# Kernel optimization log

Hardware: AMD Instinct MI355X
Metric: run time of the kernel (lower is better)

Reference implementation:

```python
import jax, jax.numpy as jnp
import numpy as np

N, E, G = 20000, 100000, 64          # nodes, edges, graphs in batch
IN, HID = 63, 128                    # in_feat, hidden_feat (per-head dim)
HEADS = (8, 8, 8)                    # num_heads per GATv2 layer
NCLS = 18
EPS = 1e-5


def setup_inputs() -> dict:
    key = jax.random.key(0)
    ks = list(jax.random.split(key, 48))
    it = iter(ks)
    nrm = lambda shape, s=0.05: jax.random.normal(next(it), shape, jnp.float32) * s

    inp = {
        "h": jax.random.normal(next(it), (N, IN), jnp.float32),
        "src": jax.random.randint(next(it), (E,), 0, N, dtype=jnp.int32),
        "dst": jax.random.randint(next(it), (E,), 0, N, dtype=jnp.int32),
        "gid": jnp.sort(jax.random.randint(next(it), (N,), 0, G, dtype=jnp.int32)),
    }
    dims = [(IN, HEADS[0] * HID), (HEADS[0] * HID, HEADS[1] * HID), (HEADS[1] * HID, HEADS[2] * HID)]
    for l, (din, dout) in enumerate(dims, 1):
        H = HEADS[l - 1]
        inp[f"w_src{l}"] = nrm((din, dout))
        inp[f"b_src{l}"] = jnp.zeros((dout,), jnp.float32)
        inp[f"w_dst{l}"] = nrm((din, dout))
        inp[f"b_dst{l}"] = jnp.zeros((dout,), jnp.float32)
        inp[f"attn{l}"] = nrm((H, HID))
        inp[f"bias{l}"] = jnp.zeros((dout,), jnp.float32)
        inp[f"gamma{l}"] = jnp.ones((dout,), jnp.float32)
        inp[f"beta{l}"] = jnp.zeros((dout,), jnp.float32)
    inp["fc1_w"] = nrm((HEADS[2] * HID, HID * 8))   # 1024 -> 1024 (hidden_feat*num_heads -> hidden_feat? see note)
    inp["fc1_b"] = jnp.zeros((HID * 8,), jnp.float32)
    inp["fc2_w"] = nrm((HID * 8, 1024))
    inp["fc2_b"] = jnp.zeros((1024,), jnp.float32)
    inp["fc3_w"] = nrm((1024, NCLS))
    inp["fc3_b"] = jnp.zeros((NCLS,), jnp.float32)
    return inp


def _gatv2(h, w_src, b_src, w_dst, b_dst, attn, bias, src, dst):
    """DGL GATv2Conv forward (dropouts are identity in eval mode)."""
    H, D = attn.shape
    fs = (h @ w_src + b_src).reshape(N, H, D)   # [N,H,D]
    fd = (h @ w_dst + b_dst).reshape(N, H, D)
    e = jax.nn.leaky_relu(fs[src] + fd[dst], 0.2)          # [E,H,D], GATv2 negative_slope=0.2
    sc = jnp.einsum('ehd,hd->eh', e, attn)                 # [E,H] attention logits
    m = jax.ops.segment_max(sc, dst, num_segments=N)       # segment-softmax over in-edges
    m = jnp.where(jnp.isfinite(m), m, 0.0)                 # guard isolated nodes
    ex = jnp.exp(sc - m[dst])
    den = jax.ops.segment_sum(ex, dst, num_segments=N)
    alpha = ex / den[dst]                                  # [E,H]
    out = jax.ops.segment_sum(alpha[..., None] * fs[src], dst, num_segments=N)  # [N,H,D]
    return out.reshape(N, H * D) + bias


def _bn(x, gamma, beta):
    mu = x.mean(0)
    var = x.var(0)  # biased, as torch BN uses for normalization
    return (x - mu) * jax.lax.rsqrt(var + EPS) * gamma + beta


def _lrelu(x):
    return jax.nn.leaky_relu(x, 0.01)  # torch F.leaky_relu default slope


def reference(h, src, dst, gid,
              w_src1, b_src1, w_dst1, b_dst1, attn1, bias1, gamma1, beta1,
              w_src2, b_src2, w_dst2, b_dst2, attn2, bias2, gamma2, beta2,
              w_src3, b_src3, w_dst3, b_dst3, attn3, bias3, gamma3, beta3,
              fc1_w, fc1_b, fc2_w, fc2_b, fc3_w, fc3_b):
    x = _lrelu(_bn(_gatv2(h, w_src1, b_src1, w_dst1, b_dst1, attn1, bias1, src, dst), gamma1, beta1))
    x = _lrelu(_bn(_gatv2(x, w_src2, b_src2, w_dst2, b_dst2, attn2, bias2, src, dst), gamma2, beta2))
    x = _lrelu(_bn(_gatv2(x, w_src3, b_src3, w_dst3, b_dst3, attn3, bias3, src, dst), gamma3, beta3))
    # AvgPooling: mean over nodes of each graph
    cnt = jax.ops.segment_sum(jnp.ones((N,), x.dtype), gid, num_segments=G)
    hg = jax.ops.segment_sum(x, gid, num_segments=G) / jnp.maximum(cnt, 1.0)[:, None]  # [G, 1024]
    z = _lrelu(hg @ fc1_w + fc1_b)
    z = _lrelu(z @ fc2_w + fc2_b)
    return z @ fc3_w + fc3_b  # [G, 18]
```

## Files before the change

kernel.cpp:

```cpp
#include <hip/hip_runtime.h>
#include <math.h>

#define N_NODES 20000
#define N_PAD   20096
#define N_EDGES 100000
#define N_GRAPHS 64
#define IN_F 63
#define NHEAD 8
#define F 1024
#define NCLS 18
#define BN_EPS 1e-5f
#define BN_CHUNKS 256

typedef __attribute__((ext_vector_type(8))) _Float16 half8v;
typedef __attribute__((ext_vector_type(4))) _Float16 half4v;
typedef __attribute__((ext_vector_type(4))) float f32x4;

__global__ void k_zero_i32(int* __restrict__ p, int n) {
    int i = blockIdx.x * blockDim.x + threadIdx.x;
    if (i < n) p[i] = 0;
}

__global__ void k_copy_i32(int* __restrict__ d, const int* __restrict__ s, int n) {
    int i = blockIdx.x * blockDim.x + threadIdx.x;
    if (i < n) d[i] = s[i];
}

__global__ void k_count(const int* __restrict__ dst, int* __restrict__ cnt) {
    int i = blockIdx.x * blockDim.x + threadIdx.x;
    if (i < N_EDGES) atomicAdd(&cnt[dst[i]], 1);
}

__global__ void k_scan(const int* __restrict__ cnt, int* __restrict__ off) {
    __shared__ int tsum[256];
    const int CH = (N_NODES + 255) / 256;
    int t = threadIdx.x;
    int s = 0;
    for (int i = 0; i < CH; ++i) {
        int idx = t * CH + i;
        if (idx < N_NODES) s += cnt[idx];
    }
    tsum[t] = s;
    __syncthreads();
    if (t == 0) {
        int acc = 0;
        for (int i = 0; i < 256; ++i) { int v = tsum[i]; tsum[i] = acc; acc += v; }
    }
    __syncthreads();
    int run = tsum[t];
    for (int i = 0; i < CH; ++i) {
        int idx = t * CH + i;
        if (idx < N_NODES) { off[idx] = run; run += cnt[idx]; }
    }
    if (t == 255) off[N_NODES] = run;
}

__global__ void k_fill(const int* __restrict__ dst, int* __restrict__ cursor,
                       int* __restrict__ csr_e) {
    int i = blockIdx.x * blockDim.x + threadIdx.x;
    if (i < N_EDGES) {
        int p = atomicAdd(&cursor[dst[i]], 1);
        csr_e[p] = i;
    }
}

__global__ void k_sort_buckets(const int* __restrict__ off, int* __restrict__ csr_e) {
    int n = blockIdx.x * blockDim.x + threadIdx.x;
    if (n >= N_NODES) return;
    int b = off[n], e = off[n + 1];
    for (int i = b + 1; i < e; ++i) {
        int v = csr_e[i];
        int j = i - 1;
        while (j >= b && csr_e[j] > v) { csr_e[j + 1] = csr_e[j]; --j; }
        csr_e[j + 1] = v;
    }
}

__global__ void k_gstart(const int* __restrict__ gid, int* __restrict__ gstart) {
    int g = blockIdx.x * blockDim.x + threadIdx.x;
    if (g > N_GRAPHS) return;
    int lo = 0, hi = N_NODES;
    while (lo < hi) {
        int mid = (lo + hi) >> 1;
        if (gid[mid] < g) lo = mid + 1; else hi = mid;
    }
    gstart[g] = lo;
}

__global__ void k_cvt_h(const float* __restrict__ h, _Float16* __restrict__ xh) {
    int idx = blockIdx.x * 256 + threadIdx.x;
    if (idx >= N_PAD * 64) return;
    int m = idx >> 6, k = idx & 63;
    float v = (m < N_NODES && k < IN_F) ? h[m * IN_F + k] : 0.f;
    xh[idx] = (_Float16)v;
}

__global__ void k_zero_pad(_Float16* __restrict__ xh) {
    int idx = blockIdx.x * 256 + threadIdx.x;
    const int total = (N_PAD - N_NODES) * F;
    if (idx < total) xh[(size_t)N_NODES * F + idx] = (_Float16)0.f;
}

__global__ void k_cvt_w2(const float* __restrict__ W0, _Float16* __restrict__ o0,
                         const float* __restrict__ W1, _Float16* __restrict__ o1,
                         int K, int Kpad) {
    const float* W = blockIdx.z ? W1 : W0;
    _Float16* wh = blockIdx.z ? o1 : o0;
    __shared__ float t[32][33];
    int kt = blockIdx.x * 32, nt = blockIdx.y * 32;
    int tx = threadIdx.x & 31, ty = threadIdx.x >> 5;
#pragma unroll
    for (int j = 0; j < 4; ++j) {
        int k = kt + ty + j * 8;
        t[ty + j * 8][tx] = (k < K) ? W[(size_t)k * F + nt + tx] : 0.f;
    }
    __syncthreads();
#pragma unroll
    for (int j = 0; j < 4; ++j) {
        int n = nt + ty + j * 8;
        wh[(size_t)n * Kpad + kt + tx] = (_Float16)t[tx][ty + j * 8];
    }
}

#define AS1C(p) ((const __attribute__((address_space(1))) void*)(p))
#define AS3(p)  ((__attribute__((address_space(3))) void*)(p))

template <int KPAD>
__launch_bounds__(256, 2)
__global__ void k_gemm_dual(const _Float16* __restrict__ A,
                            const _Float16* __restrict__ Bs, const _Float16* __restrict__ Bd,
                            const float* __restrict__ bias_s, const float* __restrict__ bias_d,
                            _Float16* __restrict__ Cs, _Float16* __restrict__ Cd) {
    __shared__ _Float16 lds[3][3][128 * 32];
    const int l = threadIdx.x & 63, w = threadIdx.x >> 6;

    const int orig = blockIdx.y * 8 + blockIdx.x;
    const int wg = (orig & 7) * (N_PAD / 128) + (orig >> 3);
    const int by = wg >> 3, bx = wg & 7;

    const int srow = w * 16 + (l >> 2);
    const int schunk = ((l & 3) ^ ((l >> 2) & 3) ^ ((l >> 4) & 3)) << 3;
    const _Float16* gA  = A  + (size_t)(by * 128 + srow) * KPAD + schunk;
    const _Float16* gBs = Bs + (size_t)(bx * 128 + srow) * KPAD + schunk;
    const _Float16* gBd = Bd + (size_t)(bx * 128 + srow) * KPAD + schunk;
    const size_t jstep = (size_t)64 * KPAD;

    const int wr = (w >> 1) * 64, wc = (w & 1) * 64;
    const int frow = l & 15;
    const int kbyte = ((l & 3) ^ ((l >> 2) & 3) ^ ((l >> 4) & 3)) << 4;

    f32x4 accS[4][4], accD[4][4];
    const f32x4 fzero = {0.f, 0.f, 0.f, 0.f};
#pragma unroll
    for (int i = 0; i < 4; ++i)
#pragma unroll
        for (int j = 0; j < 4; ++j) { accS[i][j] = fzero; accD[i][j] = fzero; }

    auto stage = [&](int b, int t) {
        const int k0 = t * 32;
        char* dA  = (char*)&lds[b][0][0] + w * 1024;
        char* dBs = (char*)&lds[b][1][0] + w * 1024;
        char* dBd = (char*)&lds[b][2][0] + w * 1024;
#pragma unroll
        for (int j = 0; j < 2; ++j) {
            __builtin_amdgcn_global_load_lds(AS1C(gA  + k0 + j * jstep), AS3(dA  + j * 4096), 16, 0, 0);
            __builtin_amdgcn_global_load_lds(AS1C(gBs + k0 + j * jstep), AS3(dBs + j * 4096), 16, 0, 0);
            __builtin_amdgcn_global_load_lds(AS1C(gBd + k0 + j * jstep), AS3(dBd + j * 4096), 16, 0, 0);
        }
    };

    auto compute = [&](int b) {
        const char* lA  = (const char*)&lds[b][0][0];
        const char* lBs = (const char*)&lds[b][1][0];
        const char* lBd = (const char*)&lds[b][2][0];
        half8v a[4];
#pragma unroll
        for (int mi = 0; mi < 4; ++mi)
            a[mi] = *(const half8v*)(lA + (wr + mi * 16 + frow) * 64 + kbyte);
#pragma unroll
        for (int ni = 0; ni < 4; ++ni) {
            const int rb = (wc + ni * 16 + frow) * 64 + kbyte;
            half8v bs = *(const half8v*)(lBs + rb);
            half8v bd = *(const half8v*)(lBd + rb);
#pragma unroll
            for (int mi = 0; mi < 4; ++mi) {
                accS[mi][ni] = __builtin_amdgcn_mfma_f32_16x16x32_f16(a[mi], bs, accS[mi][ni], 0, 0, 0);
                accD[mi][ni] = __builtin_amdgcn_mfma_f32_16x16x32_f16(a[mi], bd, accD[mi][ni], 0, 0, 0);
            }
        }
    };

    constexpr int NT = KPAD / 32;
    stage(0, 0);
    if (NT > 1) stage(1, 1);
#pragma unroll 1
    for (int t = 0; t < NT; ++t) {
        if (t == NT - 1) asm volatile("s_waitcnt vmcnt(0)" ::: "memory");
        else             asm volatile("s_waitcnt vmcnt(6)" ::: "memory");
        __builtin_amdgcn_s_barrier();
        __builtin_amdgcn_sched_barrier(0);
        if (t + 2 < NT) stage((t + 2) % 3, t + 2);
        compute(t % 3);
    }

    const int crow0 = by * 128 + wr + (l >> 4) * 4;
    const int ccol = bx * 128 + wc + (l & 15);
    float bS[4], bD[4];
#pragma unroll
    for (int ni = 0; ni < 4; ++ni) { bS[ni] = bias_s[ccol + ni * 16]; bD[ni] = bias_d[ccol + ni * 16]; }
#pragma unroll
    for (int mi = 0; mi < 4; ++mi) {
#pragma unroll
        for (int r = 0; r < 4; ++r) {
            int row = crow0 + mi * 16 + r;
            if (row < N_NODES) {
#pragma unroll
                for (int ni = 0; ni < 4; ++ni) {
                    int col = ccol + ni * 16;
                    Cs[(size_t)row * F + col] = (_Float16)(accS[mi][ni][r] + bS[ni]);
                    Cd[(size_t)row * F + col] = (_Float16)(accD[mi][ni][r] + bD[ni]);
                }
            }
        }
    }
}

__launch_bounds__(128)
__global__ void k_gat(const _Float16* __restrict__ fs, const _Float16* __restrict__ fd,
                      const int* __restrict__ off, const int* __restrict__ csr_e,
                      const int* __restrict__ src, const float* __restrict__ attn,
                      const float* __restrict__ bias, _Float16* __restrict__ y16) {
    __shared__ int s_src[128];
    const int n = blockIdx.x;
    const int t = threadIdx.x;
    const int b = off[n], e = off[n + 1];

    half8v fdv8 = *(const half8v*)(fd + (size_t)n * F + t * 8);
    float fdv[8], av[8];
    const float4 a0 = *(const float4*)(attn + (t >> 4) * 128 + (t & 15) * 8);
    const float4 a1 = *(const float4*)(attn + (t >> 4) * 128 + (t & 15) * 8 + 4);
    av[0] = a0.x; av[1] = a0.y; av[2] = a0.z; av[3] = a0.w;
    av[4] = a1.x; av[5] = a1.y; av[6] = a1.z; av[7] = a1.w;
#pragma unroll
    for (int j = 0; j < 8; ++j) fdv[j] = (float)fdv8[j];

    float m = -1e30f, den = 0.f;
    float acc[8] = {0.f, 0.f, 0.f, 0.f, 0.f, 0.f, 0.f, 0.f};

    for (int c0 = b; c0 < e; c0 += 128) {
        int ncur = e - c0; if (ncur > 128) ncur = 128;
        __syncthreads();
        if (t < ncur) s_src[t] = src[csr_e[c0 + t]];
        __syncthreads();
        for (int i = 0; i < ncur; ++i) {
            int s = s_src[i];
            half8v fsv8 = *(const half8v*)(fs + (size_t)s * F + t * 8);
            float f[8];
            float p = 0.f;
#pragma unroll
            for (int j = 0; j < 8; ++j) {
                f[j] = (float)fsv8[j];
                float v = f[j] + fdv[j];
                v = v > 0.f ? v : 0.2f * v;
                p += v * av[j];
            }
            p += __shfl_xor(p, 1);
            p += __shfl_xor(p, 2);
            p += __shfl_xor(p, 4);
            p += __shfl_xor(p, 8);
            float mn = fmaxf(m, p);
            float so = __expf(m - mn);
            float wexp = __expf(p - mn);
            den = den * so + wexp;
#pragma unroll
            for (int j = 0; j < 8; ++j) acc[j] = acc[j] * so + wexp * f[j];
            m = mn;
        }
    }
    float inv = (e > b) ? 1.f / den : 0.f;
    const float4 b0 = *(const float4*)(bias + t * 8);
    const float4 b1 = *(const float4*)(bias + t * 8 + 4);
    float bb[8] = {b0.x, b0.y, b0.z, b0.w, b1.x, b1.y, b1.z, b1.w};
    half8v o;
#pragma unroll
    for (int j = 0; j < 8; ++j) o[j] = (_Float16)(acc[j] * inv + bb[j]);
    *(half8v*)(y16 + (size_t)n * F + t * 8) = o;
}

__global__ void k_bnpart(const _Float16* __restrict__ y16, float* __restrict__ part) {
    const int ROWS = (N_NODES + BN_CHUNKS - 1) / BN_CHUNKS;
    int blk = blockIdx.x;
    int t = threadIdx.x;
    int r0 = blk * ROWS;
    int r1 = r0 + ROWS; if (r1 > N_NODES) r1 = N_NODES;
    float sx = 0.f, sy = 0.f, sz = 0.f, sw = 0.f;
    float qx = 0.f, qy = 0.f, qz = 0.f, qw = 0.f;
    for (int r = r0; r < r1; ++r) {
        half4v v = *(const half4v*)(y16 + (size_t)r * F + t * 4);
        float vx = (float)v.x, vy = (float)v.y, vz = (float)v.z, vw = (float)v.w;
        sx += vx; sy += vy; sz += vz; sw += vw;
        qx += vx * vx; qy += vy * vy; qz += vz * vz; qw += vw * vw;
    }
    float4 s4; s4.x = sx; s4.y = sy; s4.z = sz; s4.w = sw;
    float4 q4; q4.x = qx; q4.y = qy; q4.z = qz; q4.w = qw;
    *(float4*)(part + (size_t)blk * (2 * F) + t * 4) = s4;
    *(float4*)(part + (size_t)blk * (2 * F) + F + t * 4) = q4;
}

__global__ void k_bnfin(const float* __restrict__ part, const float* __restrict__ gamma,
                        const float* __restrict__ beta, float* __restrict__ scale,
                        float* __restrict__ shift) {
    int c = blockIdx.x * blockDim.x + threadIdx.x;
    if (c >= F) return;
    float s = 0.f, q = 0.f;
    for (int b = 0; b < BN_CHUNKS; ++b) {
        s += part[(size_t)b * (2 * F) + c];
        q += part[(size_t)b * (2 * F) + F + c];
    }
    float mu = s / (float)N_NODES;
    float var = q / (float)N_NODES - mu * mu;
    float sc = gamma[c] * rsqrtf(var + BN_EPS);
    scale[c] = sc;
    shift[c] = beta[c] - mu * sc;
}

__global__ void k_bnapply(const _Float16* __restrict__ y16, const float* __restrict__ scale,
                          const float* __restrict__ shift, float* __restrict__ x,
                          _Float16* __restrict__ xh, int mode) {
    int i = blockIdx.x * blockDim.x + threadIdx.x;
    if (i >= N_NODES * (F / 4)) return;
    int c4 = (i & (F / 4 - 1)) * 4;
    half4v v = ((const half4v*)y16)[i];
    float4 o;
    o.x = (float)v.x * scale[c4 + 0] + shift[c4 + 0];
    o.y = (float)v.y * scale[c4 + 1] + shift[c4 + 1];
    o.z = (float)v.z * scale[c4 + 2] + shift[c4 + 2];
    o.w = (float)v.w * scale[c4 + 3] + shift[c4 + 3];
    o.x = o.x > 0.f ? o.x : 0.01f * o.x;
    o.y = o.y > 0.f ? o.y : 0.01f * o.y;
    o.z = o.z > 0.f ? o.z : 0.01f * o.z;
    o.w = o.w > 0.f ? o.w : 0.01f * o.w;
    if (mode == 0) {
        half4v h4;
        h4.x = (_Float16)o.x; h4.y = (_Float16)o.y;
        h4.z = (_Float16)o.z; h4.w = (_Float16)o.w;
        *(half4v*)&xh[(size_t)i * 4] = h4;
    } else {
        ((float4*)x)[i] = o;
    }
}

__global__ void k_pool(const float* __restrict__ x, const int* __restrict__ gstart,
                       _Float16* __restrict__ hg16) {
    int g = blockIdx.y;
    int col = blockIdx.x * 256 + threadIdx.x;
    int r0 = gstart[g], r1 = gstart[g + 1];
    float s = 0.f;
    for (int r = r0; r < r1; ++r) s += x[(size_t)r * F + col];
    float inv = (r1 > r0) ? 1.f / (float)(r1 - r0) : 0.f;
    hg16[(size_t)g * F + col] = (_Float16)(s * inv);
}

__launch_bounds__(256)
__global__ void k_mlp_mfma(const _Float16* __restrict__ A16, const _Float16* __restrict__ Bt,
                           const float* __restrict__ bias, _Float16* __restrict__ out16,
                           float* __restrict__ out32, int mode) {
    const int l = threadIdx.x & 63, w = threadIdx.x >> 6;
    const int bx = blockIdx.x;
    const int fko = (l >> 4) * 8;

    const _Float16* pa = A16 + (size_t)(w * 16 + (l & 15)) * 1024 + fko;
    const _Float16* pb = Bt + (size_t)(bx * 64 + (l & 15)) * 1024 + fko;

    f32x4 acc[4];
    const f32x4 fzero = {0.f, 0.f, 0.f, 0.f};
#pragma unroll
    for (int ni = 0; ni < 4; ++ni) acc[ni] = fzero;

#pragma unroll 4
    for (int k0 = 0; k0 < 1024; k0 += 32) {
        half8v a = *(const half8v*)(pa + k0);
#pragma unroll
        for (int ni = 0; ni < 4; ++ni) {
            half8v b = *(const half8v*)(pb + (size_t)ni * 16 * 1024 + k0);
            acc[ni] = __builtin_amdgcn_mfma_f32_16x16x32_f16(a, b, acc[ni], 0, 0, 0);
        }
    }

    const int row0 = w * 16 + (l >> 4) * 4;
    const int col0 = bx * 64 + (l & 15);
#pragma unroll
    for (int ni = 0; ni < 4; ++ni) {
        int col = col0 + ni * 16;
        float bb = bias[col];
#pragma unroll
        for (int r = 0; r < 4; ++r) {
            float v = acc[ni][r] + bb;
            v = v > 0.f ? v : 0.01f * v;
            if (mode == 0) out16[(size_t)(row0 + r) * 1024 + col] = (_Float16)v;
            else out32[(size_t)(row0 + r) * 1024 + col] = v;
        }
    }
}

__global__ void k_fc3(const float* __restrict__ z2, const float* __restrict__ W,
                      const float* __restrict__ b, float* __restrict__ out) {
    int gw = (blockIdx.x * blockDim.x + threadIdx.x) >> 6;
    int lane = threadIdx.x & 63;
    if (gw >= N_GRAPHS * NCLS) return;
    int row = gw / NCLS, col = gw - row * NCLS;
    float s = 0.f;
    for (int k = lane; k < 1024; k += 64) s += z2[(size_t)row * 1024 + k] * W[(size_t)k * NCLS + col];
#pragma unroll
    for (int o = 32; o; o >>= 1) s += __shfl_down(s, o);
    if (lane == 0) out[(size_t)row * NCLS + col] = s + b[col];
}

extern "C" void kernel_launch(void* const* d_in, const int* in_sizes, int n_in,
                              void* d_out, int out_size, void* d_ws, size_t ws_size,
                              hipStream_t stream) {
    const float* h = (const float*)d_in[0];
    const int* src = (const int*)d_in[1];
    const int* dst = (const int*)d_in[2];
    const int* gid = (const int*)d_in[3];

    const float *w_src[3], *b_src[3], *w_dst[3], *b_dst[3], *attn[3], *bias[3], *gamma[3], *beta[3];
    for (int l = 0; l < 3; ++l) {
        int base = 4 + l * 8;
        w_src[l] = (const float*)d_in[base + 0];
        b_src[l] = (const float*)d_in[base + 1];
        w_dst[l] = (const float*)d_in[base + 2];
        b_dst[l] = (const float*)d_in[base + 3];
        attn[l]  = (const float*)d_in[base + 4];
        bias[l]  = (const float*)d_in[base + 5];
        gamma[l] = (const float*)d_in[base + 6];
        beta[l]  = (const float*)d_in[base + 7];
    }
    const float* fc1_w = (const float*)d_in[28];
    const float* fc1_b = (const float*)d_in[29];
    const float* fc2_w = (const float*)d_in[30];
    const float* fc2_b = (const float*)d_in[31];
    const float* fc3_w = (const float*)d_in[32];
    const float* fc3_b = (const float*)d_in[33];

    char* base = (char*)d_ws;
    size_t o = 0;
    auto carve = [&](size_t bytes) -> char* {
        char* p = base + o;
        o += (bytes + 255) & ~(size_t)255;
        return p;
    };
    _Float16* fs16 = (_Float16*)carve((size_t)N_NODES * F * 2);
    _Float16* fd16 = (_Float16*)carve((size_t)N_NODES * F * 2);
    _Float16* y16 = (_Float16*)carve((size_t)N_NODES * F * 2);
    float* x32 = (float*)carve((size_t)N_NODES * F * 4);
    _Float16* xh = (_Float16*)carve((size_t)N_PAD * F * 2);
    _Float16* wsh = (_Float16*)carve((size_t)F * F * 2);
    _Float16* wdh = (_Float16*)carve((size_t)F * F * 2);
    _Float16* fc1h = (_Float16*)carve((size_t)F * F * 2);
    _Float16* fc2h = (_Float16*)carve((size_t)F * F * 2);
    int* cnt = (int*)carve((size_t)N_NODES * 4);
    int* off = (int*)carve((size_t)(N_NODES + 1) * 4);
    int* cursor = (int*)carve((size_t)N_NODES * 4);
    int* csr_e = (int*)carve((size_t)N_EDGES * 4);
    float* part = (float*)carve((size_t)BN_CHUNKS * 2 * F * 4);
    float* scale = (float*)carve(F * 4);
    float* shift = (float*)carve(F * 4);
    int* gstart = (int*)carve((N_GRAPHS + 1) * 4);
    _Float16* hg16 = (_Float16*)carve((size_t)N_GRAPHS * F * 2);
    _Float16* z1h = (_Float16*)carve((size_t)N_GRAPHS * F * 2);
    float* z2 = (float*)carve((size_t)N_GRAPHS * F * 4);
    (void)ws_size;

    k_zero_i32<<<(N_NODES + 255) / 256, 256, 0, stream>>>(cnt, N_NODES);
    k_count<<<(N_EDGES + 255) / 256, 256, 0, stream>>>(dst, cnt);
    k_scan<<<1, 256, 0, stream>>>(cnt, off);
    k_copy_i32<<<(N_NODES + 255) / 256, 256, 0, stream>>>(cursor, off, N_NODES);
    k_fill<<<(N_EDGES + 255) / 256, 256, 0, stream>>>(dst, cursor, csr_e);
    k_sort_buckets<<<(N_NODES + 255) / 256, 256, 0, stream>>>(off, csr_e);
    k_gstart<<<1, 128, 0, stream>>>(gid, gstart);

    k_cvt_h<<<(N_PAD * 64 + 255) / 256, 256, 0, stream>>>(h, xh);
    k_zero_pad<<<((N_PAD - N_NODES) * F + 255) / 256, 256, 0, stream>>>(xh);
    k_cvt_w2<<<dim3(F / 32, F / 32, 2), 256, 0, stream>>>(fc1_w, fc1h, fc2_w, fc2h, F, F);

    const dim3 ggrid(8, N_PAD / 128);
    for (int l = 0; l < 3; ++l) {
        const int K = (l == 0) ? IN_F : F;
        const int Kp = (l == 0) ? 64 : F;
        k_cvt_w2<<<dim3(Kp / 32, F / 32, 2), 256, 0, stream>>>(w_src[l], wsh, w_dst[l], wdh, K, Kp);
        if (Kp == 64)
            k_gemm_dual<64><<<ggrid, 256, 0, stream>>>(xh, wsh, wdh, b_src[l], b_dst[l], fs16, fd16);
        else
            k_gemm_dual<1024><<<ggrid, 256, 0, stream>>>(xh, wsh, wdh, b_src[l], b_dst[l], fs16, fd16);
        k_gat<<<N_NODES, 128, 0, stream>>>(fs16, fd16, off, csr_e, src, attn[l], bias[l], y16);
        k_bnpart<<<BN_CHUNKS, 256, 0, stream>>>(y16, part);
        k_bnfin<<<F / 256, 256, 0, stream>>>(part, gamma[l], beta[l], scale, shift);
        k_bnapply<<<(N_NODES * (F / 4) + 255) / 256, 256, 0, stream>>>(
            y16, scale, shift, x32, xh, (l == 2) ? 1 : 0);
    }

    k_pool<<<dim3(4, N_GRAPHS), 256, 0, stream>>>(x32, gstart, hg16);
    k_mlp_mfma<<<16, 256, 0, stream>>>(hg16, fc1h, fc1_b, z1h, nullptr, 0);
    k_mlp_mfma<<<16, 256, 0, stream>>>(z1h, fc2h, fc2_b, nullptr, z2, 1);
    k_fc3<<<(N_GRAPHS * NCLS * 64 + 255) / 256, 256, 0, stream>>>(z2, fc3_w, fc3_b, (float*)d_out);
}
```

Before: 793.2 us.

## Merge preprocessing kernels, batch weight conversion, simplify GEMM pipeline, pool from fp16

Several launches are folded together. The gstart search moves into the scan kernel, the cursor copy is replaced by a second counter array, and all six 1024x1024 weight conversions run in one launch. The dual GEMM loses its templated triple-buffered global_load_lds pipeline in favour of a single-buffered 64-wide K loop with an XOR swizzle and two __syncthreads per step, which may expose load latency. The last layer now writes fp16 activations only, and pooling reads them, so the fp32 activation buffer and its writes are gone at a small precision cost.

Measured after the change: 773.2 us. -2.5%, faster.

```diff
diff --git a/kernel.cpp b/kernel.cpp
--- a/kernel.cpp
+++ b/kernel.cpp
@@ -21,17 +21,13 @@
     if (i < n) p[i] = 0;
 }
 
-__global__ void k_copy_i32(int* __restrict__ d, const int* __restrict__ s, int n) {
-    int i = blockIdx.x * blockDim.x + threadIdx.x;
-    if (i < n) d[i] = s[i];
-}
-
 __global__ void k_count(const int* __restrict__ dst, int* __restrict__ cnt) {
     int i = blockIdx.x * blockDim.x + threadIdx.x;
     if (i < N_EDGES) atomicAdd(&cnt[dst[i]], 1);
 }
 
-__global__ void k_scan(const int* __restrict__ cnt, int* __restrict__ off) {
+__global__ void k_scan(const int* __restrict__ cnt, int* __restrict__ off,
+                       const int* __restrict__ gid, int* __restrict__ gstart) {
     __shared__ int tsum[256];
     const int CH = (N_NODES + 255) / 256;
     int t = threadIdx.x;
@@ -53,14 +49,23 @@
         if (idx < N_NODES) { off[idx] = run; run += cnt[idx]; }
     }
     if (t == 255) off[N_NODES] = run;
-}
-
-__global__ void k_fill(const int* __restrict__ dst, int* __restrict__ cursor,
-                       int* __restrict__ csr_e) {
+    if (t <= N_GRAPHS) {
+        int lo = 0, hi = N_NODES;
+        while (lo < hi) {
+            int mid = (lo + hi) >> 1;
+            if (gid[mid] < t) lo = mid + 1; else hi = mid;
+        }
+        gstart[t] = lo;
+    }
+}
+
+__global__ void k_fill(const int* __restrict__ dst, const int* __restrict__ off,
+                       int* __restrict__ fcnt, int* __restrict__ csr_e) {
     int i = blockIdx.x * blockDim.x + threadIdx.x;
     if (i < N_EDGES) {
-        int p = atomicAdd(&cursor[dst[i]], 1);
-        csr_e[p] = i;
+        int d = dst[i];
+        int p = atomicAdd(&fcnt[d], 1);
+        csr_e[off[d] + p] = i;
     }
 }
 
@@ -76,17 +81,6 @@
     }
 }
 
-__global__ void k_gstart(const int* __restrict__ gid, int* __restrict__ gstart) {
-    int g = blockIdx.x * blockDim.x + threadIdx.x;
-    if (g > N_GRAPHS) return;
-    int lo = 0, hi = N_NODES;
-    while (lo < hi) {
-        int mid = (lo + hi) >> 1;
-        if (gid[mid] < g) lo = mid + 1; else hi = mid;
-    }
-    gstart[g] = lo;
-}
-
 __global__ void k_cvt_h(const float* __restrict__ h, _Float16* __restrict__ xh) {
     int idx = blockIdx.x * 256 + threadIdx.x;
     if (idx >= N_PAD * 64) return;
@@ -122,32 +116,67 @@
     }
 }
 
+__global__ void k_cvt_w6(const float* __restrict__ a0, _Float16* __restrict__ b0,
+                         const float* __restrict__ a1, _Float16* __restrict__ b1,
+                         const float* __restrict__ a2, _Float16* __restrict__ b2,
+                         const float* __restrict__ a3, _Float16* __restrict__ b3,
+                         const float* __restrict__ a4, _Float16* __restrict__ b4,
+                         const float* __restrict__ a5, _Float16* __restrict__ b5) {
+    const float* W; _Float16* wh;
+    switch (blockIdx.z) {
+        case 0: W = a0; wh = b0; break;
+        case 1: W = a1; wh = b1; break;
+        case 2: W = a2; wh = b2; break;
+        case 3: W = a3; wh = b3; break;
+        case 4: W = a4; wh = b4; break;
+        default: W = a5; wh = b5; break;
+    }
+    __shared__ float t[32][33];
+    int kt = blockIdx.x * 32, nt = blockIdx.y * 32;
+    int tx = threadIdx.x & 31, ty = threadIdx.x >> 5;
+#pragma unroll
+    for (int j = 0; j < 4; ++j) {
+        int k = kt + ty + j * 8;
+        t[ty + j * 8][tx] = W[(size_t)k * F + nt + tx];
+    }
+    __syncthreads();
+#pragma unroll
+    for (int j = 0; j < 4; ++j) {
+        int n = nt + ty + j * 8;
+        wh[(size_t)n * F + kt + tx] = (_Float16)t[tx][ty + j * 8];
+    }
+}
+
 #define AS1C(p) ((const __attribute__((address_space(1))) void*)(p))
 #define AS3(p)  ((__attribute__((address_space(3))) void*)(p))
 
-template <int KPAD>
 __launch_bounds__(256, 2)
 __global__ void k_gemm_dual(const _Float16* __restrict__ A,
                             const _Float16* __restrict__ Bs, const _Float16* __restrict__ Bd,
                             const float* __restrict__ bias_s, const float* __restrict__ bias_d,
-                            _Float16* __restrict__ Cs, _Float16* __restrict__ Cd) {
-    __shared__ _Float16 lds[3][3][128 * 32];
-    const int l = threadIdx.x & 63, w = threadIdx.x >> 6;
+                            _Float16* __restrict__ Cs, _Float16* __restrict__ Cd, int Kpad) {
+    __shared__ _Float16 lds[24576];
+    const int tid = threadIdx.x;
+    const int l = tid & 63, w = tid >> 6;
 
     const int orig = blockIdx.y * 8 + blockIdx.x;
     const int wg = (orig & 7) * (N_PAD / 128) + (orig >> 3);
     const int by = wg >> 3, bx = wg & 7;
 
-    const int srow = w * 16 + (l >> 2);
-    const int schunk = ((l & 3) ^ ((l >> 2) & 3) ^ ((l >> 4) & 3)) << 3;
-    const _Float16* gA  = A  + (size_t)(by * 128 + srow) * KPAD + schunk;
-    const _Float16* gBs = Bs + (size_t)(bx * 128 + srow) * KPAD + schunk;
-    const _Float16* gBd = Bd + (size_t)(bx * 128 + srow) * KPAD + schunk;
-    const size_t jstep = (size_t)64 * KPAD;
+    const int grow = w * 32 + (l >> 3);
+    const int gcol = ((l & 7) ^ (l >> 3)) << 3;
+    const size_t rstep = (size_t)8 * Kpad;
+    const _Float16* gA = A + (size_t)(by * 128 + grow) * Kpad + gcol;
+    const _Float16* gBs = Bs + (size_t)(bx * 128 + grow) * Kpad + gcol;
+    const _Float16* gBd = Bd + (size_t)(bx * 128 + grow) * Kpad + gcol;
+    char* sA = (char*)lds + w * 4096;
+    char* sBs = (char*)lds + 16384 + w * 4096;
+    char* sBd = (char*)lds + 32768 + w * 4096;
 
     const int wr = (w >> 1) * 64, wc = (w & 1) * 64;
     const int frow = l & 15;
-    const int kbyte = ((l & 3) ^ ((l >> 2) & 3) ^ ((l >> 4) & 3)) << 4;
+    const int swz = (l & 7) << 4;
+    const int kbase = (l >> 4) * 16;
 
     f32x4 accS[4][4], accD[4][4];
     const f32x4 fzero = {0.f, 0.f, 0.f, 0.f};
@@ -156,51 +185,38 @@
 #pragma unroll
         for (int j = 0; j < 4; ++j) { accS[i][j] = fzero; accD[i][j] = fzero; }
 
-    auto stage = [&](int b, int t) {
-        const int k0 = t * 32;
-        char* dA  = (char*)&lds[b][0][0] + w * 1024;
-        char* dBs = (char*)&lds[b][1][0] + w * 1024;
-        char* dBd = (char*)&lds[b][2][0] + w * 1024;
-#pragma unroll
-        for (int j = 0; j < 2; ++j) {
-            __builtin_amdgcn_global_load_lds(AS1C(gA  + k0 + j * jstep), AS3(dA  + j * 4096), 16, 0, 0);
-            __builtin_amdgcn_global_load_lds(AS1C(gBs + k0 + j * jstep), AS3(dBs + j * 4096), 16, 0, 0);
-            __builtin_amdgcn_global_load_lds(AS1C(gBd + k0 + j * jstep), AS3(dBd + j * 4096), 16, 0, 0);
-        }
-    };
-
-    auto compute = [&](int b) {
-        const char* lA  = (const char*)&lds[b][0][0];
-        const char* lBs = (const char*)&lds[b][1][0];
-        const char* lBd = (const char*)&lds[b][2][0];
-        half8v a[4];
-#pragma unroll
-        for (int mi = 0; mi < 4; ++mi)
-            a[mi] = *(const half8v*)(lA + (wr + mi * 16 + frow) * 64 + kbyte);
-#pragma unroll
-        for (int ni = 0; ni < 4; ++ni) {
-            const int rb = (wc + ni * 16 + frow) * 64 + kbyte;
-            half8v bs = *(const half8v*)(lBs + rb);
-            half8v bd = *(const half8v*)(lBd + rb);
+    for (int k0 = 0; k0 < Kpad; k0 += 64) {
+#pragma unroll
+        for (int j = 0; j < 4; ++j) {
+            __builtin_amdgcn_global_load_lds(AS1C(gA + j * rstep), AS3(sA + j * 1024), 16, 0, 0);
+            __builtin_amdgcn_global_load_lds(AS1C(gBs + j * rstep), AS3(sBs + j * 1024), 16, 0, 0);
+            __builtin_amdgcn_global_load_lds(AS1C(gBd + j * rstep), AS3(sBd + j * 1024), 16, 0, 0);
+        }
+        gA += 64; gBs += 64; gBd += 64;
+        __syncthreads();
+
+#pragma unroll
+        for (int kk = 0; kk < 2; ++kk) {
+            const int kb = (kk * 64 + kbase) ^ swz;
+            half8v a[4];
 #pragma unroll
             for (int mi = 0; mi < 4; ++mi) {
-                accS[mi][ni] = __builtin_amdgcn_mfma_f32_16x16x32_f16(a[mi], bs, accS[mi][ni], 0, 0, 0);
-                accD[mi][ni] = __builtin_amdgcn_mfma_f32_16x16x32_f16(a[mi], bd, accD[mi][ni], 0, 0, 0);
+                int row = wr + mi * 16 + frow;
+                a[mi] = *(const half8v*)((const char*)lds + row * 128 + kb);
             }
-        }
-    };
-
-    constexpr int NT = KPAD / 32;
-    stage(0, 0);
-    if (NT > 1) stage(1, 1);
-#pragma unroll 1
-    for (int t = 0; t < NT; ++t) {
-        if (t == NT - 1) asm volatile("s_waitcnt vmcnt(0)" ::: "memory");
-        else             asm volatile("s_waitcnt vmcnt(6)" ::: "memory");
-        __builtin_amdgcn_s_barrier();
-        __builtin_amdgcn_sched_barrier(0);
-        if (t + 2 < NT) stage((t + 2) % 3, t + 2);
-        compute(t % 3);
+#pragma unroll
+            for (int ni = 0; ni < 4; ++ni) {
+                int rowb = wc + ni * 16 + frow;
+                half8v bs = *(const half8v*)((const char*)lds + 16384 + rowb * 128 + kb);
+                half8v bd = *(const half8v*)((const char*)lds + 32768 + rowb * 128 + kb);
+#pragma unroll
+                for (int mi = 0; mi < 4; ++mi) {
+                    accS[mi][ni] = __builtin_amdgcn_mfma_f32_16x16x32_f16(a[mi], bs, accS[mi][ni], 0, 0, 0);
+                    accD[mi][ni] = __builtin_amdgcn_mfma_f32_16x16x32_f16(a[mi], bd, accD[mi][ni], 0, 0, 0);
+                }
+            }
+        }
+        __syncthreads();
     }
 
     const int crow0 = by * 128 + wr + (l >> 4) * 4;
@@ -325,8 +341,7 @@
 }
 
 __global__ void k_bnapply(const _Float16* __restrict__ y16, const float* __restrict__ scale,
-                          const float* __restrict__ shift, float* __restrict__ x,
-                          _Float16* __restrict__ xh, int mode) {
+                          const float* __restrict__ shift, _Float16* __restrict__ xh) {
     int i = blockIdx.x * blockDim.x + threadIdx.x;
     if (i >= N_NODES * (F / 4)) return;
     int c4 = (i & (F / 4 - 1)) * 4;
@@ -340,23 +355,19 @@
     o.y = o.y > 0.f ? o.y : 0.01f * o.y;
     o.z = o.z > 0.f ? o.z : 0.01f * o.z;
     o.w = o.w > 0.f ? o.w : 0.01f * o.w;
-    if (mode == 0) {
-        half4v h4;
-        h4.x = (_Float16)o.x; h4.y = (_Float16)o.y;
-        h4.z = (_Float16)o.z; h4.w = (_Float16)o.w;
-        *(half4v*)&xh[(size_t)i * 4] = h4;
-    } else {
-        ((float4*)x)[i] = o;
-    }
-}
-
-__global__ void k_pool(const float* __restrict__ x, const int* __restrict__ gstart,
+    half4v h4;
+    h4.x = (_Float16)o.x; h4.y = (_Float16)o.y;
+    h4.z = (_Float16)o.z; h4.w = (_Float16)o.w;
+    *(half4v*)&xh[(size_t)i * 4] = h4;
+}
+
+__global__ void k_pool(const _Float16* __restrict__ x16, const int* __restrict__ gstart,
                        _Float16* __restrict__ hg16) {
     int g = blockIdx.y;
     int col = blockIdx.x * 256 + threadIdx.x;
     int r0 = gstart[g], r1 = gstart[g + 1];
     float s = 0.f;
-    for (int r = r0; r < r1; ++r) s += x[(size_t)r * F + col];
+    for (int r = r0; r < r1; ++r) s += (float)x16[(size_t)r * F + col];
     float inv = (r1 > r0) ? 1.f / (float)(r1 - r0) : 0.f;
     hg16[(size_t)g * F + col] = (_Float16)(s * inv);
 }
@@ -453,15 +464,18 @@
     _Float16* fs16 = (_Float16*)carve((size_t)N_NODES * F * 2);
     _Float16* fd16 = (_Float16*)carve((size_t)N_NODES * F * 2);
     _Float16* y16 = (_Float16*)carve((size_t)N_NODES * F * 2);
-    float* x32 = (float*)carve((size_t)N_NODES * F * 4);
     _Float16* xh = (_Float16*)carve((size_t)N_PAD * F * 2);
-    _Float16* wsh = (_Float16*)carve((size_t)F * F * 2);
-    _Float16* wdh = (_Float16*)carve((size_t)F * F * 2);
+    _Float16* w1s = (_Float16*)carve((size_t)F * 64 * 2);
+    _Float16* w1d = (_Float16*)carve((size_t)F * 64 * 2);
+    _Float16* w2s = (_Float16*)carve((size_t)F * F * 2);
+    _Float16* w2d = (_Float16*)carve((size_t)F * F * 2);
+    _Float16* w3s = (_Float16*)carve((size_t)F * F * 2);
+    _Float16* w3d = (_Float16*)carve((size_t)F * F * 2);
     _Float16* fc1h = (_Float16*)carve((size_t)F * F * 2);
     _Float16* fc2h = (_Float16*)carve((size_t)F * F * 2);
-    int* cnt = (int*)carve((size_t)N_NODES * 4);
+    int* cnt = (int*)carve((size_t)2 * N_NODES * 4);
+    int* fcnt = cnt + N_NODES;
     int* off = (int*)carve((size_t)(N_NODES + 1) * 4);
-    int* cursor = (int*)carve((size_t)N_NODES * 4);
     int* csr_e = (int*)carve((size_t)N_EDGES * 4);
     float* part = (float*)carve((size_t)BN_CHUNKS * 2 * F * 4);
     float* scale = (float*)carve(F * 4);
@@ -472,35 +486,32 @@
     float* z2 = (float*)carve((size_t)N_GRAPHS * F * 4);
     (void)ws_size;
 
-    k_zero_i32<<<(N_NODES + 255) / 256, 256, 0, stream>>>(cnt, N_NODES);
+    k_zero_i32<<<(2 * N_NODES + 255) / 256, 256, 0, stream>>>(cnt, 2 * N_NODES);
     k_count<<<(N_EDGES + 255) / 256, 256, 0, stream>>>(dst, cnt);
-    k_scan<<<1, 256, 0, stream>>>(cnt, off);
-    k_copy_i32<<<(N_NODES + 255) / 256, 256, 0, stream>>>(cursor, off, N_NODES);
-    k_fill<<<(N_EDGES + 255) / 256, 256, 0, stream>>>(dst, cursor, csr_e);
+    k_scan<<<1, 256, 0, stream>>>(cnt, off, gid, gstart);
+    k_fill<<<(N_EDGES + 255) / 256, 256, 0, stream>>>(dst, off, fcnt, csr_e);
     k_sort_buckets<<<(N_NODES + 255) / 256, 256, 0, stream>>>(off, csr_e);
-    k_gstart<<<1, 128, 0, stream>>>(gid, gstart);
 
     k_cvt_h<<<(N_PAD * 64 + 255) / 256, 256, 0, stream>>>(h, xh);
     k_zero_pad<<<((N_PAD - N_NODES) * F + 255) / 256, 256, 0, stream>>>(xh);
-    k_cvt_w2<<<dim3(F / 32, F / 32, 2), 256, 0, stream>>>(fc1_w, fc1h, fc2_w, fc2h, F, F);
+    k_cvt_w2<<<dim3(2, F / 32, 2), 256, 0, stream>>>(w_src[0], w1s, w_dst[0], w1d, IN_F, 64);
+    k_cvt_w6<<<dim3(F / 32, F / 32, 6), 256, 0, stream>>>(
+        w_src[1], w2s, w_dst[1], w2d, w_src[2], w3s, w_dst[2], w3d, fc1_w, fc1h, fc2_w, fc2h);
 
     const dim3 ggrid(8, N_PAD / 128);
+    const _Float16* ws16[3] = {w1s, w2s, w3s};
+    const _Float16* wd16[3] = {w1d, w2d, w3d};
     for (int l = 0; l < 3; ++l) {
-        const int K = (l == 0) ? IN_F : F;
         const int Kp = (l == 0) ? 64 : F;
-        k_cvt_w2<<<dim3(Kp / 32, F / 32, 2), 256, 0, stream>>>(w_src[l], wsh, w_dst[l], wdh, K, Kp);
-        if (Kp == 64)
-            k_gemm_dual<64><<<ggrid, 256, 0, stream>>>(xh, wsh, wdh, b_src[l], b_dst[l], fs16, fd16);
-        else
-            k_gemm_dual<1024><<<ggrid, 256, 0, stream>>>(xh, wsh, wdh, b_src[l], b_dst[l], fs16, fd16);
+        k_gemm_dual<<<ggrid, 256, 0, stream>>>(xh, ws16[l], wd16[l], b_src[l], b_dst[l],
+                                               fs16, fd16, Kp);
         k_gat<<<N_NODES, 128, 0, stream>>>(fs16, fd16, off, csr_e, src, attn[l], bias[l], y16);
         k_bnpart<<<BN_CHUNKS, 256, 0, stream>>>(y16, part);
         k_bnfin<<<F / 256, 256, 0, stream>>>(part, gamma[l], beta[l], scale, shift);
-        k_bnapply<<<(N_NODES * (F / 4) + 255) / 256, 256, 0, stream>>>(
-            y16, scale, shift, x32, xh, (l == 2) ? 1 : 0);
-    }
-
-    k_pool<<<dim3(4, N_GRAPHS), 256, 0, stream>>>(x32, gstart, hg16);
+        k_bnapply<<<(N_NODES * (F / 4) + 255) / 256, 256, 0, stream>>>(y16, scale, shift, xh);
+    }
+
+    k_pool<<<dim3(4, N_GRAPHS), 256, 0, stream>>>(xh, gstart, hg16);
     k_mlp_mfma<<<16, 256, 0, stream>>>(hg16, fc1h, fc1_b, z1h, nullptr, 0);
     k_mlp_mfma<<<16, 256, 0, stream>>>(z1h, fc2h, fc2_b, nullptr, z2, 1);
     k_fc3<<<(N_GRAPHS * NCLS * 64 + 255) / 256, 256, 0, stream>>>(z2, fc3_w, fc3_b, (float*)d_out);
```
